# Performance work log

Hardware: AMD Instinct MI355X
Metric: run time of the kernel (lower is better)

Reference implementation:

```python
import jax, jax.numpy as jnp
import numpy as np

K = 20
NEG = 0.2      # leaky relu slope
EPS = 1e-5     # layernorm eps


def knn(x, k=K):
    # x: [B, C, N] -> neighbor indices [B, N, k] by largest negative sq-distance
    xt = jnp.swapaxes(x, 1, 2)                      # [B, N, C]
    inner = -2.0 * jnp.einsum('bnc,bcm->bnm', xt, x)
    xx = jnp.sum(x * x, axis=1)                     # [B, N]
    pd = -xx[:, :, None] - inner - xx[:, None, :]   # [B, N, N]
    _, idx = jax.lax.top_k(pd, k)
    return idx


def graph_feature(x, k=K):
    # x: [B, C, N] -> edge features [B, 2C, N, k] = cat(neighbor - center, center)
    xt = jnp.swapaxes(x, 1, 2)                      # [B, N, C]
    idx = knn(x, k)                                 # [B, N, k]
    nbr = jax.vmap(lambda f, i: f[i])(xt, idx)      # [B, N, k, C]
    ctr = jnp.broadcast_to(xt[:, :, None, :], nbr.shape)
    feat = jnp.concatenate([nbr - ctr, ctr], axis=-1)
    return jnp.transpose(feat, (0, 3, 1, 2))


def lrelu(x):
    return jnp.where(x >= 0, x, NEG * x)


def conv1x1(x, w):
    # x: [B, C, N, k], w: [O, C]  (BatchNorm2d in eval with default stats == identity)
    return jnp.einsum('oc,bcnk->bonk', w, x)


def layernorm(x, g, b):
    m = jnp.mean(x, axis=-1, keepdims=True)
    v = jnp.var(x, axis=-1, keepdims=True)
    return (x - m) * jax.lax.rsqrt(v + EPS) * g + b


def l2n(x):
    return x / jnp.linalg.norm(x, axis=1, keepdims=True)


def fc_layer(x, w, bias, g, beta):
    # l2-normalize -> Linear -> LayerNorm -> LeakyReLU (fc_layer with norm=True, bn=True)
    x = l2n(x)
    x = x @ w.T
    if bias is not None:
        x = x + bias
    return lrelu(layernorm(x, g, beta))


def transform_net(f0, tw1, tw2, tw3, tfc1_w, tfc1_g, tfc1_b, tfc2_w, tfc2_bias, tfc2_g, tfc2_b, tfc3_w, tfc3_b):
    # f0: [B, 6, N, k]
    h = lrelu(conv1x1(f0, tw1))                     # [B, 64, N, k]
    h = lrelu(conv1x1(h, tw2))                      # [B, 128, N, k]
    h = jnp.max(h, axis=-1, keepdims=True)          # [B, 128, N, 1]
    h = lrelu(conv1x1(h, tw3))                      # [B, 1024, N, 1]
    h = jnp.max(h, axis=2)[:, :, 0]                 # [B, 1024]
    h = fc_layer(h, tfc1_w, None, tfc1_g, tfc1_b)   # dgcnn: fc1 bias=False
    h = fc_layer(h, tfc2_w, tfc2_bias, tfc2_g, tfc2_b)
    h = h @ tfc3_w.T + tfc3_b                       # [B, 9]
    h = h + jnp.eye(3, dtype=h.dtype).reshape(9)
    return h.reshape(-1, 3, 3)


def setup_inputs() -> dict:
    key = jax.random.key(0)
    ks = jax.random.split(key, 16)

    def w(k, o, i):
        return jax.random.normal(k, (o, i), dtype=jnp.float32) / np.sqrt(i)

    inp = {
        'x': jax.random.normal(ks[0], (16, 3, 1024), dtype=jnp.float32),
        # transform_net params
        'tw1': w(ks[1], 64, 6),
        'tw2': w(ks[2], 128, 64),
        'tw3': w(ks[3], 1024, 128),
        'tfc1_w': w(ks[4], 512, 1024),
        'tfc1_g': jnp.ones((512,), jnp.float32),
        'tfc1_b': jnp.zeros((512,), jnp.float32),
        'tfc2_w': w(ks[5], 256, 512),
        'tfc2_bias': jnp.zeros((256,), jnp.float32),
        'tfc2_g': jnp.ones((256,), jnp.float32),
        'tfc2_b': jnp.zeros((256,), jnp.float32),
        'tfc3_w': w(ks[6], 9, 256) * 0.01,
        'tfc3_b': jnp.zeros((9,), jnp.float32),
        # EdgeConv params (1x1 convs, bias=False for dgcnn)
        'w1': w(ks[7], 64, 6),
        'w2': w(ks[8], 64, 128),
        'w3': w(ks[9], 128, 128),
        'w4': w(ks[10], 256, 256),
        'w5': w(ks[11], 1024, 512),
    }
    return inp


def reference(x, tw1, tw2, tw3, tfc1_w, tfc1_g, tfc1_b, tfc2_w, tfc2_bias, tfc2_g, tfc2_b,
              tfc3_w, tfc3_b, w1, w2, w3, w4, w5):
    # spatial transform from first graph feature
    f0 = graph_feature(x)                           # [B, 6, N, k]
    t = transform_net(f0, tw1, tw2, tw3, tfc1_w, tfc1_g, tfc1_b,
                      tfc2_w, tfc2_bias, tfc2_g, tfc2_b, tfc3_w, tfc3_b)
    x = jnp.einsum('bij,bjn->bin', t, x)            # [B, 3, N]

    # 4 EdgeConv blocks: graph_feature -> 1x1 conv (+BN identity) -> lrelu -> max over k
    x1 = jnp.max(lrelu(conv1x1(graph_feature(x), w1)), axis=-1)    # [B, 64, N]
    x2 = jnp.max(lrelu(conv1x1(graph_feature(x1), w2)), axis=-1)   # [B, 64, N]
    x3 = jnp.max(lrelu(conv1x1(graph_feature(x2), w3)), axis=-1)   # [B, 128, N]
    x4 = jnp.max(lrelu(conv1x1(graph_feature(x3), w4)), axis=-1)   # [B, 256, N]

    xc = jnp.concatenate([x1, x2, x3, x4], axis=1)  # [B, 512, N]
    x5 = lrelu(jnp.einsum('oc,bcn->bon', w5, xc))   # [B, 1024, N]
    return jnp.max(x5, axis=-1)                     # [B, 1024] global feature
```

## Files before the change

### kernel.cpp

```cpp
#include <hip/hip_runtime.h>
#include <math.h>

#define BATCH 16
#define NPTS 1024
#define KNN 20

__device__ __forceinline__ float lrelu(float v) { return v >= 0.f ? v : 0.2f * v; }

typedef __attribute__((ext_vector_type(8))) short bf16x8;
typedef __attribute__((ext_vector_type(4))) float f32x4;
typedef unsigned long long ull;

__device__ __forceinline__ ushort f2bf(float f) {
  union { float f; unsigned u; } v; v.f = f;
  unsigned r = (v.u + 0x7FFFu + ((v.u >> 16) & 1u)) >> 16;
  return (ushort)r;
}

__device__ __forceinline__ unsigned wave_min_u32(unsigned v) {
  unsigned t;
  t = (unsigned)__builtin_amdgcn_update_dpp((int)v, (int)v, 0x111, 0xf, 0xf, false);
  v = t < v ? t : v;
  t = (unsigned)__builtin_amdgcn_update_dpp((int)v, (int)v, 0x112, 0xf, 0xf, false);
  v = t < v ? t : v;
  t = (unsigned)__builtin_amdgcn_update_dpp((int)v, (int)v, 0x114, 0xf, 0xf, false);
  v = t < v ? t : v;
  t = (unsigned)__builtin_amdgcn_update_dpp((int)v, (int)v, 0x118, 0xf, 0xf, false);
  v = t < v ? t : v;
  t = (unsigned)__builtin_amdgcn_update_dpp((int)v, (int)v, 0x142, 0xf, 0xf, false);
  v = t < v ? t : v;
  t = (unsigned)__builtin_amdgcn_update_dpp((int)v, (int)v, 0x143, 0xf, 0xf, false);
  v = t < v ? t : v;
  return (unsigned)__builtin_amdgcn_readlane((int)v, 63);
}

__global__ __launch_bounds__(256)
void wsplit_t_kernel(const float* __restrict__ W, float* __restrict__ waT,
                     float* __restrict__ wdT, int O, int Cc) {
  int e = blockIdx.x * 256 + threadIdx.x;
  if (e < O * Cc) {
    int c = e / O, o = e - c * O;
    float a = W[o * 2 * Cc + c], bb = W[o * 2 * Cc + Cc + c];
    waT[e] = a; wdT[e] = bb - a;
  }
}

__global__ __launch_bounds__(256)
void wsplit_bf_kernel(const float* __restrict__ W, ushort* __restrict__ wa_bf,
                      ushort* __restrict__ wd_bf, int O, int Cc) {
  int e = blockIdx.x * 256 + threadIdx.x;
  if (e < O * Cc) {
    int o = e / Cc, c = e - o * Cc;
    float a = W[o * 2 * Cc + c], bb = W[o * 2 * Cc + Cc + c];
    wa_bf[e] = f2bf(a); wd_bf[e] = f2bf(bb - a);
  }
}

__global__ __launch_bounds__(256)
void cvt_bf16_kernel(const float* __restrict__ in, ushort* __restrict__ outp, int n) {
  int e = blockIdx.x * 256 + threadIdx.x;
  if (e < n) outp[e] = f2bf(in[e]);
}

__global__ __launch_bounds__(256)
void wtrans_kernel(const float* __restrict__ W, float* __restrict__ wT, int O, int Cc) {
  int e = blockIdx.x * 256 + threadIdx.x;
  if (e < O * Cc) {
    int c = e / O, o = e - c * O;
    wT[e] = W[(size_t)o * Cc + c];
  }
}

__global__ __launch_bounds__(256)
void xx3_kernel(const float* __restrict__ x, float* __restrict__ xx) {
  const int b = blockIdx.y;
  const int n = blockIdx.x * 256 + threadIdx.x;
  const float* xb = x + (size_t)b * 3 * NPTS;
  float a = xb[n], bb = xb[NPTS + n], c = xb[2 * NPTS + n];
  xx[b * NPTS + n] = a * a + bb * bb + c * c;
}

template<int C>
__global__ __launch_bounds__(256)
void knn_cn_kernel(const float* __restrict__ Xt, long sb,
                   const float* __restrict__ xx, int* __restrict__ idxout) {
  __shared__ float sc4[4][NPTS];
  const int b = blockIdx.y, i0 = blockIdx.x * 8;
  const int tid = threadIdx.x;
  const float* Xb = Xt + (size_t)b * sb;
  const int j0 = tid * 4;
  float acc[8][4];
  #pragma unroll
  for (int q = 0; q < 8; ++q)
    #pragma unroll
    for (int u = 0; u < 4; ++u) acc[q][u] = 0.f;
  for (int c = 0; c < C; ++c) {
    const float4 xv = *reinterpret_cast<const float4*>(Xb + (size_t)c * NPTS + j0);
    const float* xr = Xb + (size_t)c * NPTS + i0;
    #pragma unroll
    for (int q = 0; q < 8; ++q) {
      const float xiq = xr[q];
      acc[q][0] = fmaf(xiq, xv.x, acc[q][0]);
      acc[q][1] = fmaf(xiq, xv.y, acc[q][1]);
      acc[q][2] = fmaf(xiq, xv.z, acc[q][2]);
      acc[q][3] = fmaf(xiq, xv.w, acc[q][3]);
    }
  }
  const float4 xxj = *reinterpret_cast<const float4*>(xx + b * NPTS + j0);
  const int wv = tid >> 6, lane = tid & 63;
  unsigned ku0[16], ku1[16];

  #pragma unroll
  for (int q = 0; q < 4; ++q) {
    float4 st;
    st.x = fmaf(-2.f, acc[q][0], xxj.x);
    st.y = fmaf(-2.f, acc[q][1], xxj.y);
    st.z = fmaf(-2.f, acc[q][2], xxj.z);
    st.w = fmaf(-2.f, acc[q][3], xxj.w);
    *reinterpret_cast<float4*>(&sc4[q][j0]) = st;
  }
  __syncthreads();
  #pragma unroll
  for (int s = 0; s < 16; ++s) {
    const unsigned u = __float_as_uint(sc4[wv][lane + 64 * s]);
    ku0[s] = u ^ ((unsigned)((int)u >> 31) | 0x80000000u);
  }
  __syncthreads();
  #pragma unroll
  for (int q = 4; q < 8; ++q) {
    float4 st;
    st.x = fmaf(-2.f, acc[q][0], xxj.x);
    st.y = fmaf(-2.f, acc[q][1], xxj.y);
    st.z = fmaf(-2.f, acc[q][2], xxj.z);
    st.w = fmaf(-2.f, acc[q][3], xxj.w);
    *reinterpret_cast<float4*>(&sc4[q - 4][j0]) = st;
  }
  __syncthreads();
  #pragma unroll
  for (int s = 0; s < 16; ++s) {
    const unsigned u = __float_as_uint(sc4[wv][lane + 64 * s]);
    ku1[s] = u ^ ((unsigned)((int)u >> 31) | 0x80000000u);
  }

  unsigned b1v0 = 0xFFFFFFFFu, b2v0 = 0xFFFFFFFFu; int b1s0 = 0, b2s0 = 0;
  unsigned b1v1 = 0xFFFFFFFFu, b2v1 = 0xFFFFFFFFu; int b1s1 = 0, b2s1 = 0;
  #pragma unroll
  for (int s = 0; s < 16; ++s) {
    const unsigned s0 = ku0[s], s1 = ku1[s];
    const bool a1 = s0 < b1v0, a2 = s0 < b2v0;
    const unsigned na1 = a1 ? s0 : b1v0;  const int nas1 = a1 ? s : b1s0;
    const unsigned na2 = a1 ? b1v0 : (a2 ? s0 : b2v0);
    const int nas2 = a1 ? b1s0 : (a2 ? s : b2s0);
    b1v0 = na1; b1s0 = nas1; b2v0 = na2; b2s0 = nas2;
    const bool c1c = s1 < b1v1, c2c = s1 < b2v1;
    const unsigned nc1 = c1c ? s1 : b1v1;  const int ncs1 = c1c ? s : b1s1;
    const unsigned nc2 = c1c ? b1v1 : (c2c ? s1 : b2v1);
    const int ncs2 = c1c ? b1s1 : (c2c ? s : b2s1);
    b1v1 = nc1; b1s1 = ncs1; b2v1 = nc2; b2s1 = ncs2;
  }
  const unsigned INVS = 0xFFFFFFFFu;
  unsigned c1s0 = b1v0, c2s0 = b2v0;  int c1j0 = lane + (b1s0 << 6), c2j0 = lane + (b2s0 << 6);
  unsigned c1s1 = b1v1, c2s1 = b2v1;  int c1j1 = lane + (b1s1 << 6), c2j1 = lane + (b2s1 << 6);

  int my0 = 0, my1 = 0;
  for (int t = 0; t < KNN; ++t) {
    const unsigned ws0 = wave_min_u32(c1s0);
    const unsigned ws1 = wave_min_u32(c1s1);
    const int wl0 = __ffsll((long long)__ballot(c1s0 == ws0)) - 1;
    const int wl1 = __ffsll((long long)__ballot(c1s1 == ws1)) - 1;
    const int jw0 = __builtin_amdgcn_readlane(c1j0, wl0);
    const int jw1 = __builtin_amdgcn_readlane(c1j1, wl1);
    if (lane == t) { my0 = jw0; my1 = jw1; }
    const bool win0 = (lane == wl0), win1 = (lane == wl1);
    c1s0 = win0 ? c2s0 : c1s0;  c1j0 = win0 ? c2j0 : c1j0;  c2s0 = win0 ? INVS : c2s0;
    c1s1 = win1 ? c2s1 : c1s1;  c1j1 = win1 ? c2j1 : c1j1;  c2s1 = win1 ? INVS : c2s1;
    if (__any((c1s0 == INVS) || (c1s1 == INVS))) {
      if (c1s0 == INVS) {
        unsigned m1 = INVS, m2 = INVS; int r1 = 0, r2 = 0;
        #pragma unroll
        for (int s = 0; s < 16; ++s) {
          const unsigned k = ku0[s];
          const bool ok = k > ws0;
          const bool a1 = ok && (k < m1), a2 = ok && (k < m2);
          const unsigned nm1 = a1 ? k : m1;  const int nr1 = a1 ? s : r1;
          const unsigned nm2 = a1 ? m1 : (a2 ? k : m2);
          const int nr2 = a1 ? r1 : (a2 ? s : r2);
          m1 = nm1; r1 = nr1; m2 = nm2; r2 = nr2;
        }
        c1s0 = (m1 == INVS) ? 0xFFFFFFFEu : m1;  c1j0 = lane + (r1 << 6);
        c2s0 = (m2 == INVS) ? 0xFFFFFFFEu : m2;  c2j0 = lane + (r2 << 6);
      }
      if (c1s1 == INVS) {
        unsigned m1 = INVS, m2 = INVS; int r1 = 0, r2 = 0;
        #pragma unroll
        for (int s = 0; s < 16; ++s) {
          const unsigned k = ku1[s];
          const bool ok = k > ws1;
          const bool a1 = ok && (k < m1), a2 = ok && (k < m2);
          const unsigned nm1 = a1 ? k : m1;  const int nr1 = a1 ? s : r1;
          const unsigned nm2 = a1 ? m1 : (a2 ? k : m2);
          const int nr2 = a1 ? r1 : (a2 ? s : r2);
          m1 = nm1; r1 = nr1; m2 = nm2; r2 = nr2;
        }
        c1s1 = (m1 == INVS) ? 0xFFFFFFFEu : m1;  c1j1 = lane + (r1 << 6);
        c2s1 = (m2 == INVS) ? 0xFFFFFFFEu : m2;  c2j1 = lane + (r2 << 6);
      }
    }
  }
  if (lane < KNN) {
    idxout[(size_t)(b * NPTS + i0 + wv) * KNN + lane] = my0;
    idxout[(size_t)(b * NPTS + i0 + wv + 4) * KNN + lane] = my1;
  }
}

__global__ __launch_bounds__(256)
void gemm_kernel(const float* __restrict__ X, long sxb, int sxn, int sxc,
                 const float* __restrict__ WT, int ldW, int C,
                 float* __restrict__ out, int sob, int son) {
  __shared__ __align__(16) float Xs[16][64];
  __shared__ __align__(16) float Ws[16][64];
  const int b = blockIdx.z;
  const int n0 = blockIdx.x * 64, o0 = blockIdx.y * 64;
  const int tid = threadIdx.x;
  const int lr = tid & 63;
  const int c4 = (tid >> 6) * 4;
  const int tn = tid & 15, to = tid >> 4;
  float acc[4][4];
  #pragma unroll
  for (int i = 0; i < 4; ++i)
    #pragma unroll
    for (int j = 0; j < 4; ++j) acc[i][j] = 0.f;

  const size_t xbase = (size_t)b * sxb;
  for (int k0 = 0; k0 < C; k0 += 16) {
    #pragma unroll
    for (int u = 0; u < 4; ++u) {
      int c = k0 + c4 + u;
      float xv = 0.f, wv = 0.f;
      if (c < C) {
        xv = X[xbase + (size_t)(n0 + lr) * sxn + (size_t)c * sxc];
        wv = WT[(size_t)c * ldW + o0 + lr];
      }
      Xs[c4 + u][lr] = xv;
      Ws[c4 + u][lr] = wv;
    }
    __syncthreads();
    #pragma unroll
    for (int kk = 0; kk < 16; ++kk) {
      const float4 xa = *reinterpret_cast<const float4*>(&Xs[kk][tn * 4]);
      const float4 wb = *reinterpret_cast<const float4*>(&Ws[kk][to * 4]);
      const float xr[4] = {xa.x, xa.y, xa.z, xa.w};
      const float wr[4] = {wb.x, wb.y, wb.z, wb.w};
      #pragma unroll
      for (int i = 0; i < 4; ++i)
        #pragma unroll
        for (int j = 0; j < 4; ++j) acc[i][j] = fmaf(xr[i], wr[j], acc[i][j]);
    }
    __syncthreads();
  }
  #pragma unroll
  for (int i = 0; i < 4; ++i) {
    float4 st = make_float4(acc[i][0], acc[i][1], acc[i][2], acc[i][3]);
    *reinterpret_cast<float4*>(&out[(size_t)b * sob + (size_t)(n0 + tn * 4 + i) * son + o0 + to * 4]) = st;
  }
}

template<int EPI>
__global__ __launch_bounds__(256)
void gemm128_kernel(const float* __restrict__ X, long sxb, int scN,
                    const float* __restrict__ WT, int ldW, int C,
                    float* __restrict__ out, int sob, int son, int snb) {
  __shared__ __align__(16) float Xs[16][128];
  __shared__ __align__(16) float Ws[16][128];
  __shared__ __align__(16) float red[16][132];
  const int b = blockIdx.z;
  const int n0 = blockIdx.x * 128, o0 = blockIdx.y * 128;
  const int tid = threadIdx.x;
  const int tn = tid & 15, to = tid >> 4;
  float acc[8][8];
  #pragma unroll
  for (int i = 0; i < 8; ++i)
    #pragma unroll
    for (int j = 0; j < 8; ++j) acc[i][j] = 0.f;

  const size_t xbase = (size_t)b * sxb;
  for (int c0 = 0; c0 < C; c0 += 16) {
    #pragma unroll
    for (int it = 0; it < 2; ++it) {
      const int task = tid + it * 256;
      const int kk = task >> 5, n4 = (task & 31) * 4;
      *reinterpret_cast<float4*>(&Xs[kk][n4]) =
        *reinterpret_cast<const float4*>(&X[xbase + (size_t)(c0 + kk) * scN + n0 + n4]);
      *reinterpret_cast<float4*>(&Ws[kk][n4]) =
        *reinterpret_cast<const float4*>(&WT[(size_t)(c0 + kk) * ldW + o0 + n4]);
    }
    __syncthreads();
    #pragma unroll
    for (int kk = 0; kk < 16; ++kk) {
      const float4 xa0 = *reinterpret_cast<const float4*>(&Xs[kk][tn * 4]);
      const float4 xa1 = *reinterpret_cast<const float4*>(&Xs[kk][64 + tn * 4]);
      const float4 wb0 = *reinterpret_cast<const float4*>(&Ws[kk][to * 4]);
      const float4 wb1 = *reinterpret_cast<const float4*>(&Ws[kk][64 + to * 4]);
      const float xr[8] = {xa0.x, xa0.y, xa0.z, xa0.w, xa1.x, xa1.y, xa1.z, xa1.w};
      const float wr[8] = {wb0.x, wb0.y, wb0.z, wb0.w, wb1.x, wb1.y, wb1.z, wb1.w};
      #pragma unroll
      for (int i = 0; i < 8; ++i)
        #pragma unroll
        for (int j = 0; j < 8; ++j) acc[i][j] = fmaf(xr[i], wr[j], acc[i][j]);
    }
    __syncthreads();
  }

  if (EPI == 0) {
    #pragma unroll
    for (int i = 0; i < 8; ++i) {
      const int n = n0 + (i >> 2) * 64 + tn * 4 + (i & 3);
      float4 s0 = make_float4(acc[i][0], acc[i][1], acc[i][2], acc[i][3]);
      float4 s1 = make_float4(acc[i][4], acc[i][5], acc[i][6], acc[i][7]);
      *reinterpret_cast<float4*>(&out[(size_t)b * sob + (size_t)n * son + o0 + to * 4]) = s0;
      *reinterpret_cast<float4*>(&out[(size_t)b * sob + (size_t)n * son + o0 + 64 + to * 4]) = s1;
    }
  } else {
    #pragma unroll
    for (int j = 0; j < 8; ++j) {
      float m = lrelu(acc[0][j]);
      #pragma unroll
      for (int i = 1; i < 8; ++i) m = fmaxf(m, lrelu(acc[i][j]));
      red[tn][(j >> 2) * 64 + to * 4 + (j & 3)] = m;
    }
    __syncthreads();
    if (tid < 128) {
      float m = red[0][tid];
      #pragma unroll
      for (int t = 1; t < 16; ++t) m = fmaxf(m, red[t][tid]);
      out[(size_t)b * sob + (size_t)blockIdx.x * snb + o0 + tid] = m;
    }
  }
}

template<int EPI>
__global__ __launch_bounds__(256)
void gemm_mfma_kernel(const ushort* __restrict__ Xg, long sxb, int ldX,
                      const ushort* __restrict__ Wg, int ldW, int K,
                      float* __restrict__ out, long sob, int son, int snb) {
  __shared__ __align__(16) ushort As[128 * 64];
  __shared__ __align__(16) ushort Bs[128 * 64];
// ... 150 lines not shown
  #pragma unroll
  for (int it = 0; it < 5; ++it) {
    const int task = tid + it * 256;
    const int e = task >> 4, cq = (task & 15) * 4;
    const int p = e / KNN, t = e - p * KNN;
    const int j = idxs[p][t];
    const float4 yv = *reinterpret_cast<const float4*>(&ya[(size_t)(b * NPTS + j) * 64 + cq]);
    const float4 zv = *reinterpret_cast<const float4*>(&zbs[p][cq]);
    float4 hv;
    hv.x = lrelu(yv.x + zv.x); hv.y = lrelu(yv.y + zv.y);
    hv.z = lrelu(yv.z + zv.z); hv.w = lrelu(yv.w + zv.w);
    *reinterpret_cast<float4*>(&h1s[e][cq]) = hv;
  }
  __syncthreads();

  const int eg = tid >> 4, og = tid & 15;
  float acc[5][8];
  #pragma unroll
  for (int u = 0; u < 5; ++u)
    #pragma unroll
    for (int v = 0; v < 8; ++v) acc[u][v] = 0.f;
  #pragma unroll 4
  for (int kk = 0; kk < 64; ++kk) {
    float hv[5];
    #pragma unroll
    for (int u = 0; u < 5; ++u) hv[u] = h1s[eg * 5 + u][kk];
    const float4 w0 = *reinterpret_cast<const float4*>(&ws[kk][og * 4]);
    const float4 w1 = *reinterpret_cast<const float4*>(&ws[kk][64 + og * 4]);
    const float wr[8] = {w0.x, w0.y, w0.z, w0.w, w1.x, w1.y, w1.z, w1.w};
    #pragma unroll
    for (int u = 0; u < 5; ++u)
      #pragma unroll
      for (int v = 0; v < 8; ++v) acc[u][v] = fmaf(hv[u], wr[v], acc[u][v]);
  }

  const int p = eg >> 2, d = eg & 3;
  float m[8];
  #pragma unroll
  for (int v = 0; v < 8; ++v) {
    float mm = lrelu(acc[0][v]);
    #pragma unroll
    for (int u = 1; u < 5; ++u) mm = fmaxf(mm, lrelu(acc[u][v]));
    mm = fmaxf(mm, __shfl_xor(mm, 16));
    mm = fmaxf(mm, __shfl_xor(mm, 32));
    m[v] = mm;
  }
  if (d == 0) {
    #pragma unroll
    for (int v = 0; v < 8; ++v) {
      const int o = og * 4 + (v & 3) + (v >> 2) * 64;
      ot[o][p] = m[v];
    }
  }
  __syncthreads();
  if (tid < 128) {
    float4 st = make_float4(ot[tid][0], ot[tid][1], ot[tid][2], ot[tid][3]);
    *reinterpret_cast<float4*>(&h2m[(size_t)(b * 128 + tid) * NPTS + i0]) = st;
  }
}

__global__ __launch_bounds__(256)
void reduce_max_kernel(const float* __restrict__ part, float* __restrict__ outp, int nt) {
  const int b = blockIdx.y;
  const int o = blockIdx.x * 256 + threadIdx.x;
  float m = part[(size_t)(b * nt) * 1024 + o];
  for (int t = 1; t < nt; ++t) m = fmaxf(m, part[(size_t)(b * nt + t) * 1024 + o]);
  outp[b * 1024 + o] = m;
}

__device__ __forceinline__ float block_reduce_sum(float v, float* rbuf) {
  #pragma unroll
  for (int off = 32; off > 0; off >>= 1) v += __shfl_xor(v, off);
  const int w = threadIdx.x >> 6, lane = threadIdx.x & 63;
  const int nw = blockDim.x >> 6;
  if (lane == 0) rbuf[w] = v;
  __syncthreads();
  float tot = 0.f;
  for (int i = 0; i < nw; ++i) tot += rbuf[i];
  __syncthreads();
  return tot;
}

__global__ __launch_bounds__(256)
void fc1_kernel(const float* __restrict__ gin_g, const float* __restrict__ Wt,
                const float* __restrict__ gam, const float* __restrict__ bet,
                float* __restrict__ outp) {
  __shared__ __align__(16) float gin[1024];
  __shared__ float hbuf[512];
  __shared__ float rbuf[8];
  const int b = blockIdx.x, tid = threadIdx.x;
  for (int e = tid; e < 1024; e += 256) gin[e] = gin_g[b * 1024 + e];
  __syncthreads();
  float ps = 0.f;
  for (int e = tid; e < 1024; e += 256) ps = fmaf(gin[e], gin[e], ps);
  float ss = block_reduce_sum(ps, rbuf);
  float rinv = 1.0f / sqrtf(ss);
  #pragma unroll
  for (int r = 0; r < 2; ++r) {
    int o = tid + r * 256;
    const float* wrow = Wt + (size_t)o * 1024;
    float a = 0.f;
    for (int c4 = 0; c4 < 256; ++c4) {
      float4 wv = *reinterpret_cast<const float4*>(wrow + c4 * 4);
      float4 gv = *reinterpret_cast<const float4*>(&gin[c4 * 4]);
      a = fmaf(wv.x, gv.x, a); a = fmaf(wv.y, gv.y, a);
      a = fmaf(wv.z, gv.z, a); a = fmaf(wv.w, gv.w, a);
    }
    hbuf[o] = a * rinv;
  }
  __syncthreads();
  float pm = hbuf[tid] + hbuf[tid + 256];
  float mean = block_reduce_sum(pm, rbuf) * (1.f / 512.f);
  float d0 = hbuf[tid] - mean, d1 = hbuf[tid + 256] - mean;
  float var = block_reduce_sum(d0 * d0 + d1 * d1, rbuf) * (1.f / 512.f);
  float rs = 1.0f / sqrtf(var + 1e-5f);
  #pragma unroll
  for (int r = 0; r < 2; ++r) {
    int o = tid + r * 256;
    float yv = (hbuf[o] - mean) * rs * gam[o] + bet[o];
    outp[b * 512 + o] = lrelu(yv);
  }
}

__global__ __launch_bounds__(256)
void fc2_kernel(const float* __restrict__ inp, const float* __restrict__ Wt,
                const float* __restrict__ bias, const float* __restrict__ gam,
                const float* __restrict__ bet, float* __restrict__ outp) {
  __shared__ __align__(16) float gin[512];
  __shared__ float rbuf[8];
  const int b = blockIdx.x, tid = threadIdx.x;
  for (int e = tid; e < 512; e += 256) gin[e] = inp[b * 512 + e];
  __syncthreads();
  float ps = 0.f;
  for (int e = tid; e < 512; e += 256) ps = fmaf(gin[e], gin[e], ps);
  float ss = block_reduce_sum(ps, rbuf);
  float rinv = 1.0f / sqrtf(ss);
  const float* wrow = Wt + (size_t)tid * 512;
  float a = 0.f;
  for (int c4 = 0; c4 < 128; ++c4) {
    float4 wv = *reinterpret_cast<const float4*>(wrow + c4 * 4);
    float4 gv = *reinterpret_cast<const float4*>(&gin[c4 * 4]);
    a = fmaf(wv.x, gv.x, a); a = fmaf(wv.y, gv.y, a);
    a = fmaf(wv.z, gv.z, a); a = fmaf(wv.w, gv.w, a);
  }
  a = a * rinv + bias[tid];
  float mean = block_reduce_sum(a, rbuf) * (1.f / 256.f);
  float d = a - mean;
  float var = block_reduce_sum(d * d, rbuf) * (1.f / 256.f);
  float rs = 1.0f / sqrtf(var + 1e-5f);
  float yv = (a - mean) * rs * gam[tid] + bet[tid];
  outp[b * 256 + tid] = lrelu(yv);
}

__global__ __launch_bounds__(64)
void fc3_kernel(const float* __restrict__ inp, const float* __restrict__ Wt,
                const float* __restrict__ bias, float* __restrict__ tmat) {
  __shared__ float gin[256];
  const int b = blockIdx.x, tid = threadIdx.x;
  for (int e = tid; e < 256; e += 64) gin[e] = inp[b * 256 + e];
  __syncthreads();
  if (tid < 9) {
    const float* wrow = Wt + tid * 256;
    float a = 0.f;
    for (int c = 0; c < 256; ++c) a = fmaf(wrow[c], gin[c], a);
    a += bias[tid];
    if (tid == 0 || tid == 4 || tid == 8) a += 1.f;
    tmat[b * 9 + tid] = a;
  }
}

__global__ __launch_bounds__(256)
void xform_kernel(const float* __restrict__ x, const float* __restrict__ tmat,
                  float* __restrict__ xt) {
  const int b = blockIdx.y;
  const int n = blockIdx.x * 256 + threadIdx.x;
  const float* xb = x + (size_t)b * 3 * NPTS;
  const float x0 = xb[n], x1 = xb[NPTS + n], x2 = xb[2 * NPTS + n];
  const float* t = tmat + b * 9;
  float* ob = xt + (size_t)b * 3 * NPTS;
  #pragma unroll
  for (int i = 0; i < 3; ++i)
    ob[i * NPTS + n] = fmaf(t[3 * i], x0, fmaf(t[3 * i + 1], x1, t[3 * i + 2] * x2));
}

extern "C" void kernel_launch(void* const* d_in, const int* in_sizes, int n_in,
                              void* d_out, int out_size, void* d_ws, size_t ws_size,
                              hipStream_t stream) {
  (void)in_sizes; (void)n_in; (void)out_size; (void)ws_size;
  const float* x       = (const float*)d_in[0];
  const float* tw1     = (const float*)d_in[1];
  const float* tw2     = (const float*)d_in[2];
  const float* tw3     = (const float*)d_in[3];
  const float* tfc1_w  = (const float*)d_in[4];
  const float* tfc1_g  = (const float*)d_in[5];
  const float* tfc1_b  = (const float*)d_in[6];
  const float* tfc2_w  = (const float*)d_in[7];
  const float* tfc2_bias = (const float*)d_in[8];
  const float* tfc2_g  = (const float*)d_in[9];
  const float* tfc2_b  = (const float*)d_in[10];
  const float* tfc3_w  = (const float*)d_in[11];
  const float* tfc3_b  = (const float*)d_in[12];
  const float* w1      = (const float*)d_in[13];
  const float* w2      = (const float*)d_in[14];
  const float* w3      = (const float*)d_in[15];
  const float* w4      = (const float*)d_in[16];
  const float* w5      = (const float*)d_in[17];
  float* out = (float*)d_out;

  char* wsb = (char*)d_ws;
  size_t off = 0;
  auto alloc = [&](size_t bytes) -> void* {
    void* p = wsb + off;
    off += (bytes + 255) & ~(size_t)255;
    return p;
  };
  float* ybuf = (float*)alloc((size_t)BATCH * NPTS * 256 * 4);
  float* zbuf = (float*)alloc((size_t)BATCH * NPTS * 256 * 4);
  float* xcT  = (float*)alloc((size_t)BATCH * 512 * NPTS * 4);
  ushort* xc_bf = (ushort*)alloc((size_t)BATCH * NPTS * 512 * 2);
  float* h2m  = (float*)alloc((size_t)BATCH * 128 * NPTS * 4);
  float* part = (float*)alloc((size_t)BATCH * 16 * 1024 * 4);
  int*   idxb = (int*)alloc((size_t)BATCH * NPTS * KNN * 4);
  float* xxb  = (float*)alloc((size_t)BATCH * NPTS * 4);
  float* xt   = (float*)alloc((size_t)BATCH * 3 * NPTS * 4);
  float* gbuf = (float*)alloc((size_t)BATCH * 1024 * 4);
  float* f1o  = (float*)alloc((size_t)BATCH * 512 * 4);
  float* f2o  = (float*)alloc((size_t)BATCH * 256 * 4);
  float* tmat = (float*)alloc((size_t)BATCH * 9 * 4);
  float* tw1aT = (float*)alloc(3 * 64 * 4);
  float* tw1dT = (float*)alloc(3 * 64 * 4);
  float* w1aT  = (float*)alloc(3 * 64 * 4);
  float* w1dT  = (float*)alloc(3 * 64 * 4);
  float* w2aT  = (float*)alloc(64 * 64 * 4);
  float* w2dT  = (float*)alloc(64 * 64 * 4);
  float* w3aT  = (float*)alloc(64 * 128 * 4);
  float* w3dT  = (float*)alloc(64 * 128 * 4);
  ushort* w4a_bf = (ushort*)alloc(256 * 128 * 2);
  ushort* w4d_bf = (ushort*)alloc(256 * 128 * 2);
  ushort* w5_bf  = (ushort*)alloc(1024 * 512 * 2);
  float* tw2T  = (float*)alloc(64 * 128 * 4);
  float* tw3T  = (float*)alloc(128 * 1024 * 4);

  wsplit_t_kernel<<<1, 256, 0, stream>>>(tw1, tw1aT, tw1dT, 64, 3);
  wsplit_t_kernel<<<1, 256, 0, stream>>>(w1, w1aT, w1dT, 64, 3);
  wsplit_t_kernel<<<16, 256, 0, stream>>>(w2, w2aT, w2dT, 64, 64);
  wsplit_t_kernel<<<32, 256, 0, stream>>>(w3, w3aT, w3dT, 128, 64);
  wsplit_bf_kernel<<<128, 256, 0, stream>>>(w4, w4a_bf, w4d_bf, 256, 128);
  cvt_bf16_kernel<<<2048, 256, 0, stream>>>(w5, w5_bf, 1024 * 512);
  wtrans_kernel<<<32, 256, 0, stream>>>(tw2, tw2T, 128, 64);
  wtrans_kernel<<<512, 256, 0, stream>>>(tw3, tw3T, 1024, 128);

  xx3_kernel<<<dim3(4, 16), 256, 0, stream>>>(x, xxb);
  knn_cn_kernel<3><<<dim3(128, 16), 256, 0, stream>>>(x, 3 * NPTS, xxb, idxb);
  gemm_kernel<<<dim3(16, 1, 16), 256, 0, stream>>>(x, 3 * NPTS, 1, NPTS, tw1aT, 64, 3,
                                                   ybuf, NPTS * 64, 64);
  gemm_kernel<<<dim3(16, 1, 16), 256, 0, stream>>>(x, 3 * NPTS, 1, NPTS, tw1dT, 64, 3,
                                                   zbuf, NPTS * 64, 64);
  h12_gemm_kernel<<<dim3(256, 16), 256, 0, stream>>>(ybuf, zbuf, idxb, tw2T, h2m);
  gemm128_kernel<1><<<dim3(8, 8, 16), 256, 0, stream>>>(h2m, 128 * NPTS, NPTS, tw3T, 1024, 128,
                                                        part, 8 * 1024, 0, 1024);
  reduce_max_kernel<<<dim3(4, 16), 256, 0, stream>>>(part, gbuf, 8);
  fc1_kernel<<<16, 256, 0, stream>>>(gbuf, tfc1_w, tfc1_g, tfc1_b, f1o);
  fc2_kernel<<<16, 256, 0, stream>>>(f1o, tfc2_w, tfc2_bias, tfc2_g, tfc2_b, f2o);
  fc3_kernel<<<16, 64, 0, stream>>>(f2o, tfc3_w, tfc3_b, tmat);
  xform_kernel<<<dim3(4, 16), 256, 0, stream>>>(x, tmat, xt);

  xx3_kernel<<<dim3(4, 16), 256, 0, stream>>>(xt, xxb);
  knn_cn_kernel<3><<<dim3(128, 16), 256, 0, stream>>>(xt, 3 * NPTS, xxb, idxb);
  gemm_kernel<<<dim3(16, 1, 16), 256, 0, stream>>>(xt, 3 * NPTS, 1, NPTS, w1aT, 64, 3,
                                                   ybuf, NPTS * 64, 64);
  gemm_kernel<<<dim3(16, 1, 16), 256, 0, stream>>>(xt, 3 * NPTS, 1, NPTS, w1dT, 64, 3,
                                                   zbuf, NPTS * 64, 64);
  edge_max_cn_kernel<64, 64><<<dim3(16, 16), 256, 0, stream>>>(ybuf, zbuf, idxb, xcT, xxb,
                                                               xc_bf, 0);

  knn_cn_kernel<64><<<dim3(128, 16), 256, 0, stream>>>(xcT, 512 * NPTS, xxb, idxb);
  gemm_kernel<<<dim3(16, 1, 16), 256, 0, stream>>>(xcT, 512 * NPTS, 1, NPTS, w2aT, 64, 64,
                                                   ybuf, NPTS * 64, 64);
  gemm_kernel<<<dim3(16, 1, 16), 256, 0, stream>>>(xcT, 512 * NPTS, 1, NPTS, w2dT, 64, 64,
                                                   zbuf, NPTS * 64, 64);
  edge_max_cn_kernel<64, 64><<<dim3(16, 16), 256, 0, stream>>>(ybuf, zbuf, idxb,
                                                               xcT + 64 * NPTS, xxb, xc_bf, 64);

  knn_cn_kernel<64><<<dim3(128, 16), 256, 0, stream>>>(xcT + 64 * NPTS, 512 * NPTS, xxb, idxb);
  gemm_kernel<<<dim3(16, 2, 16), 256, 0, stream>>>(xcT + 64 * NPTS, 512 * NPTS, 1, NPTS,
                                                   w3aT, 128, 64, ybuf, NPTS * 128, 128);
  gemm_kernel<<<dim3(16, 2, 16), 256, 0, stream>>>(xcT + 64 * NPTS, 512 * NPTS, 1, NPTS,
                                                   w3dT, 128, 64, zbuf, NPTS * 128, 128);
  edge_max_cn_kernel<128, 64><<<dim3(16, 16), 256, 0, stream>>>(ybuf, zbuf, idxb,
                                                                xcT + 128 * NPTS, xxb, xc_bf, 128);

  knn_cn_kernel<128><<<dim3(128, 16), 256, 0, stream>>>(xcT + 128 * NPTS, 512 * NPTS, xxb, idxb);
  gemm_mfma_kernel<0><<<dim3(8, 2, 16), 256, 0, stream>>>(xc_bf + 128, (long)NPTS * 512, 512,
                                                          w4a_bf, 128, 128,
                                                          ybuf, (long)NPTS * 256, 256, 0);
  gemm_mfma_kernel<0><<<dim3(8, 2, 16), 256, 0, stream>>>(xc_bf + 128, (long)NPTS * 512, 512,
                                                          w4d_bf, 128, 128,
                                                          zbuf, (long)NPTS * 256, 256, 0);
  edge_max_cn_kernel<256, 32><<<dim3(32, 16), 256, 0, stream>>>(ybuf, zbuf, idxb,
                                                                xcT + 256 * NPTS, nullptr,
                                                                xc_bf, 256);

  gemm_mfma_kernel<1><<<dim3(8, 8, 16), 256, 0, stream>>>(xc_bf, (long)NPTS * 512, 512,
                                                          w5_bf, 512, 512,
                                                          part, 8 * 1024, 0, 1024);
  reduce_max_kernel<<<dim3(4, 16), 256, 0, stream>>>(part, out, 8);
}
```

Before: 755.4 us.

## Widen kNN tile to 16 rows, fuse dual 1x1 GEMMs and FC chain

```diff
diff --git a/kernel.cpp b/kernel.cpp
--- a/kernel.cpp
+++ b/kernel.cpp
@@ -85,20 +85,20 @@
 void knn_cn_kernel(const float* __restrict__ Xt, long sb,
                    const float* __restrict__ xx, int* __restrict__ idxout) {
   __shared__ float sc4[4][NPTS];
-  const int b = blockIdx.y, i0 = blockIdx.x * 8;
+  const int b = blockIdx.y, i0 = blockIdx.x * 16;
   const int tid = threadIdx.x;
   const float* Xb = Xt + (size_t)b * sb;
   const int j0 = tid * 4;
-  float acc[8][4];
-  #pragma unroll
-  for (int q = 0; q < 8; ++q)
+  float acc[16][4];
+  #pragma unroll
+  for (int q = 0; q < 16; ++q)
     #pragma unroll
     for (int u = 0; u < 4; ++u) acc[q][u] = 0.f;
   for (int c = 0; c < C; ++c) {
     const float4 xv = *reinterpret_cast<const float4*>(Xb + (size_t)c * NPTS + j0);
     const float* xr = Xb + (size_t)c * NPTS + i0;
     #pragma unroll
-    for (int q = 0; q < 8; ++q) {
+    for (int q = 0; q < 16; ++q) {
       const float xiq = xr[q];
       acc[q][0] = fmaf(xiq, xv.x, acc[q][0]);
       acc[q][1] = fmaf(xiq, xv.y, acc[q][1]);
@@ -108,160 +108,158 @@
   }
   const float4 xxj = *reinterpret_cast<const float4*>(xx + b * NPTS + j0);
   const int wv = tid >> 6, lane = tid & 63;
-  unsigned ku0[16], ku1[16];
-
-  #pragma unroll
-  for (int q = 0; q < 4; ++q) {
-    float4 st;
-    st.x = fmaf(-2.f, acc[q][0], xxj.x);
-    st.y = fmaf(-2.f, acc[q][1], xxj.y);
-    st.z = fmaf(-2.f, acc[q][2], xxj.z);
-    st.w = fmaf(-2.f, acc[q][3], xxj.w);
-    *reinterpret_cast<float4*>(&sc4[q][j0]) = st;
-  }
-  __syncthreads();
-  #pragma unroll
-  for (int s = 0; s < 16; ++s) {
-    const unsigned u = __float_as_uint(sc4[wv][lane + 64 * s]);
-    ku0[s] = u ^ ((unsigned)((int)u >> 31) | 0x80000000u);
-  }
-  __syncthreads();
-  #pragma unroll
-  for (int q = 4; q < 8; ++q) {
-    float4 st;
-    st.x = fmaf(-2.f, acc[q][0], xxj.x);
-    st.y = fmaf(-2.f, acc[q][1], xxj.y);
-    st.z = fmaf(-2.f, acc[q][2], xxj.z);
-    st.w = fmaf(-2.f, acc[q][3], xxj.w);
-    *reinterpret_cast<float4*>(&sc4[q - 4][j0]) = st;
-  }
-  __syncthreads();
-  #pragma unroll
-  for (int s = 0; s < 16; ++s) {
-    const unsigned u = __float_as_uint(sc4[wv][lane + 64 * s]);
-    ku1[s] = u ^ ((unsigned)((int)u >> 31) | 0x80000000u);
-  }
-
-  unsigned b1v0 = 0xFFFFFFFFu, b2v0 = 0xFFFFFFFFu; int b1s0 = 0, b2s0 = 0;
-  unsigned b1v1 = 0xFFFFFFFFu, b2v1 = 0xFFFFFFFFu; int b1s1 = 0, b2s1 = 0;
-  #pragma unroll
-  for (int s = 0; s < 16; ++s) {
-    const unsigned s0 = ku0[s], s1 = ku1[s];
-    const bool a1 = s0 < b1v0, a2 = s0 < b2v0;
-    const unsigned na1 = a1 ? s0 : b1v0;  const int nas1 = a1 ? s : b1s0;
-    const unsigned na2 = a1 ? b1v0 : (a2 ? s0 : b2v0);
-    const int nas2 = a1 ? b1s0 : (a2 ? s : b2s0);
-    b1v0 = na1; b1s0 = nas1; b2v0 = na2; b2s0 = nas2;
-    const bool c1c = s1 < b1v1, c2c = s1 < b2v1;
-    const unsigned nc1 = c1c ? s1 : b1v1;  const int ncs1 = c1c ? s : b1s1;
-    const unsigned nc2 = c1c ? b1v1 : (c2c ? s1 : b2v1);
-    const int ncs2 = c1c ? b1s1 : (c2c ? s : b2s1);
-    b1v1 = nc1; b1s1 = ncs1; b2v1 = nc2; b2s1 = ncs2;
+  unsigned ku[4][16];
+
+  #pragma unroll
+  for (int r = 0; r < 4; ++r) {
+    if (r > 0) __syncthreads();
+    #pragma unroll
+    for (int q = 0; q < 4; ++q) {
+      const int qq = r * 4 + q;
+      float4 st;
+      st.x = fmaf(-2.f, acc[qq][0], xxj.x);
+      st.y = fmaf(-2.f, acc[qq][1], xxj.y);
+      st.z = fmaf(-2.f, acc[qq][2], xxj.z);
+      st.w = fmaf(-2.f, acc[qq][3], xxj.w);
+      *reinterpret_cast<float4*>(&sc4[q][j0]) = st;
+    }
+    __syncthreads();
+    #pragma unroll
+    for (int s = 0; s < 16; ++s) {
+      const unsigned u = __float_as_uint(sc4[wv][lane + 64 * s]);
+      ku[r][s] = u ^ ((unsigned)((int)u >> 31) | 0x80000000u);
+    }
+  }
+
+  unsigned c1s[4], c2s[4]; int c1j[4], c2j[4];
+  #pragma unroll
+  for (int r = 0; r < 4; ++r) {
+    unsigned b1 = 0xFFFFFFFFu, b2 = 0xFFFFFFFFu; int s1 = 0, s2 = 0;
+    #pragma unroll
+    for (int s = 0; s < 16; ++s) {
+      const unsigned k = ku[r][s];
+      const bool a1 = k < b1, a2 = k < b2;
+      const unsigned n1 = a1 ? k : b1;  const int ns1 = a1 ? s : s1;
+      const unsigned n2 = a1 ? b1 : (a2 ? k : b2);
+      const int ns2 = a1 ? s1 : (a2 ? s : s2);
+      b1 = n1; s1 = ns1; b2 = n2; s2 = ns2;
+    }
+    c1s[r] = b1; c1j[r] = lane + (s1 << 6);
+    c2s[r] = b2; c2j[r] = lane + (s2 << 6);
   }
   const unsigned INVS = 0xFFFFFFFFu;
-  unsigned c1s0 = b1v0, c2s0 = b2v0;  int c1j0 = lane + (b1s0 << 6), c2j0 = lane + (b2s0 << 6);
-  unsigned c1s1 = b1v1, c2s1 = b2v1;  int c1j1 = lane + (b1s1 << 6), c2j1 = lane + (b2s1 << 6);
-
-  int my0 = 0, my1 = 0;
+  int my[4] = {0, 0, 0, 0};
   for (int t = 0; t < KNN; ++t) {
-    const unsigned ws0 = wave_min_u32(c1s0);
-    const unsigned ws1 = wave_min_u32(c1s1);
-    const int wl0 = __ffsll((long long)__ballot(c1s0 == ws0)) - 1;
-    const int wl1 = __ffsll((long long)__ballot(c1s1 == ws1)) - 1;
-    const int jw0 = __builtin_amdgcn_readlane(c1j0, wl0);
-    const int jw1 = __builtin_amdgcn_readlane(c1j1, wl1);
-    if (lane == t) { my0 = jw0; my1 = jw1; }
-    const bool win0 = (lane == wl0), win1 = (lane == wl1);
-    c1s0 = win0 ? c2s0 : c1s0;  c1j0 = win0 ? c2j0 : c1j0;  c2s0 = win0 ? INVS : c2s0;
-    c1s1 = win1 ? c2s1 : c1s1;  c1j1 = win1 ? c2j1 : c1j1;  c2s1 = win1 ? INVS : c2s1;
-    if (__any((c1s0 == INVS) || (c1s1 == INVS))) {
-      if (c1s0 == INVS) {
-        unsigned m1 = INVS, m2 = INVS; int r1 = 0, r2 = 0;
-        #pragma unroll
-        for (int s = 0; s < 16; ++s) {
-          const unsigned k = ku0[s];
-          const bool ok = k > ws0;
-          const bool a1 = ok && (k < m1), a2 = ok && (k < m2);
-          const unsigned nm1 = a1 ? k : m1;  const int nr1 = a1 ? s : r1;
-          const unsigned nm2 = a1 ? m1 : (a2 ? k : m2);
-          const int nr2 = a1 ? r1 : (a2 ? s : r2);
-          m1 = nm1; r1 = nr1; m2 = nm2; r2 = nr2;
+    unsigned ws[4]; int wl[4], jw[4];
+    #pragma unroll
+    for (int r = 0; r < 4; ++r) ws[r] = wave_min_u32(c1s[r]);
+    #pragma unroll
+    for (int r = 0; r < 4; ++r) wl[r] = __ffsll((long long)__ballot(c1s[r] == ws[r])) - 1;
+    #pragma unroll
+    for (int r = 0; r < 4; ++r) jw[r] = __builtin_amdgcn_readlane(c1j[r], wl[r]);
+    if (lane == t) {
+      #pragma unroll
+      for (int r = 0; r < 4; ++r) my[r] = jw[r];
+    }
+    bool cons = false;
+    #pragma unroll
+    for (int r = 0; r < 4; ++r) {
+      const bool win = (lane == wl[r]);
+      c1s[r] = win ? c2s[r] : c1s[r];
+      c1j[r] = win ? c2j[r] : c1j[r];
+      c2s[r] = win ? INVS : c2s[r];
+      cons = cons || (c1s[r] == INVS);
+    }
+    if (__any(cons)) {
+      #pragma unroll
+      for (int r = 0; r < 4; ++r) {
+        if (c1s[r] == INVS) {
+          unsigned m1 = INVS, m2 = INVS; int r1 = 0, r2 = 0;
+          #pragma unroll
+          for (int s = 0; s < 16; ++s) {
+            const unsigned k = ku[r][s];
+            const bool ok = k > ws[r];
+            const bool a1 = ok && (k < m1), a2 = ok && (k < m2);
+            const unsigned nm1 = a1 ? k : m1;  const int nr1 = a1 ? s : r1;
+            const unsigned nm2 = a1 ? m1 : (a2 ? k : m2);
+            const int nr2 = a1 ? r1 : (a2 ? s : r2);
+            m1 = nm1; r1 = nr1; m2 = nm2; r2 = nr2;
+          }
+          c1s[r] = (m1 == INVS) ? 0xFFFFFFFEu : m1;  c1j[r] = lane + (r1 << 6);
+          c2s[r] = (m2 == INVS) ? 0xFFFFFFFEu : m2;  c2j[r] = lane + (r2 << 6);
         }
-        c1s0 = (m1 == INVS) ? 0xFFFFFFFEu : m1;  c1j0 = lane + (r1 << 6);
-        c2s0 = (m2 == INVS) ? 0xFFFFFFFEu : m2;  c2j0 = lane + (r2 << 6);
       }
-      if (c1s1 == INVS) {
-        unsigned m1 = INVS, m2 = INVS; int r1 = 0, r2 = 0;
-        #pragma unroll
-        for (int s = 0; s < 16; ++s) {
-          const unsigned k = ku1[s];
-          const bool ok = k > ws1;
-          const bool a1 = ok && (k < m1), a2 = ok && (k < m2);
-          const unsigned nm1 = a1 ? k : m1;  const int nr1 = a1 ? s : r1;
-          const unsigned nm2 = a1 ? m1 : (a2 ? k : m2);
-          const int nr2 = a1 ? r1 : (a2 ? s : r2);
-          m1 = nm1; r1 = nr1; m2 = nm2; r2 = nr2;
-        }
-        c1s1 = (m1 == INVS) ? 0xFFFFFFFEu : m1;  c1j1 = lane + (r1 << 6);
-        c2s1 = (m2 == INVS) ? 0xFFFFFFFEu : m2;  c2j1 = lane + (r2 << 6);
-      }
     }
   }
   if (lane < KNN) {
-    idxout[(size_t)(b * NPTS + i0 + wv) * KNN + lane] = my0;
-    idxout[(size_t)(b * NPTS + i0 + wv + 4) * KNN + lane] = my1;
-  }
-}
-
-__global__ __launch_bounds__(256)
-void gemm_kernel(const float* __restrict__ X, long sxb, int sxn, int sxc,
-                 const float* __restrict__ WT, int ldW, int C,
-                 float* __restrict__ out, int sob, int son) {
+    #pragma unroll
+    for (int r = 0; r < 4; ++r)
+      idxout[(size_t)(b * NPTS + i0 + r * 4 + wv) * KNN + lane] = my[r];
+  }
+}
+
+__global__ __launch_bounds__(256)
+void gemm_dual_kernel(const float* __restrict__ X, long sxb, int sxn, int sxc,
+                      const float* __restrict__ WaT, const float* __restrict__ WdT,
+                      int ldW, int C,
+                      float* __restrict__ outY, float* __restrict__ outZ,
+                      int sob, int son) {
   __shared__ __align__(16) float Xs[16][64];
-  __shared__ __align__(16) float Ws[16][64];
+  __shared__ __align__(16) float Was[16][64];
+  __shared__ __align__(16) float Wds[16][64];
   const int b = blockIdx.z;
   const int n0 = blockIdx.x * 64, o0 = blockIdx.y * 64;
   const int tid = threadIdx.x;
   const int lr = tid & 63;
   const int c4 = (tid >> 6) * 4;
   const int tn = tid & 15, to = tid >> 4;
-  float acc[4][4];
+  float accY[4][4], accZ[4][4];
   #pragma unroll
   for (int i = 0; i < 4; ++i)
     #pragma unroll
-    for (int j = 0; j < 4; ++j) acc[i][j] = 0.f;
+    for (int j = 0; j < 4; ++j) { accY[i][j] = 0.f; accZ[i][j] = 0.f; }
 
   const size_t xbase = (size_t)b * sxb;
   for (int k0 = 0; k0 < C; k0 += 16) {
     #pragma unroll
     for (int u = 0; u < 4; ++u) {
       int c = k0 + c4 + u;
-      float xv = 0.f, wv = 0.f;
+      float xv = 0.f, wa = 0.f, wd = 0.f;
       if (c < C) {
         xv = X[xbase + (size_t)(n0 + lr) * sxn + (size_t)c * sxc];
-        wv = WT[(size_t)c * ldW + o0 + lr];
+        wa = WaT[(size_t)c * ldW + o0 + lr];
+        wd = WdT[(size_t)c * ldW + o0 + lr];
       }
       Xs[c4 + u][lr] = xv;
-      Ws[c4 + u][lr] = wv;
+      Was[c4 + u][lr] = wa;
+      Wds[c4 + u][lr] = wd;
     }
     __syncthreads();
     #pragma unroll
     for (int kk = 0; kk < 16; ++kk) {
       const float4 xa = *reinterpret_cast<const float4*>(&Xs[kk][tn * 4]);
-      const float4 wb = *reinterpret_cast<const float4*>(&Ws[kk][to * 4]);
+      const float4 wav = *reinterpret_cast<const float4*>(&Was[kk][to * 4]);
+      const float4 wdv = *reinterpret_cast<const float4*>(&Wds[kk][to * 4]);
       const float xr[4] = {xa.x, xa.y, xa.z, xa.w};
-      const float wr[4] = {wb.x, wb.y, wb.z, wb.w};
+      const float war[4] = {wav.x, wav.y, wav.z, wav.w};
+      const float wdr[4] = {wdv.x, wdv.y, wdv.z, wdv.w};
       #pragma unroll
       for (int i = 0; i < 4; ++i)
         #pragma unroll
-        for (int j = 0; j < 4; ++j) acc[i][j] = fmaf(xr[i], wr[j], acc[i][j]);
+        for (int j = 0; j < 4; ++j) {
+          accY[i][j] = fmaf(xr[i], war[j], accY[i][j]);
+          accZ[i][j] = fmaf(xr[i], wdr[j], accZ[i][j]);
+        }
     }
     __syncthreads();
   }
   #pragma unroll
   for (int i = 0; i < 4; ++i) {
-    float4 st = make_float4(acc[i][0], acc[i][1], acc[i][2], acc[i][3]);
-    *reinterpret_cast<float4*>(&out[(size_t)b * sob + (size_t)(n0 + tn * 4 + i) * son + o0 + to * 4]) = st;
+    const size_t base = (size_t)b * sob + (size_t)(n0 + tn * 4 + i) * son + o0 + to * 4;
+    *reinterpret_cast<float4*>(&outY[base]) =
+      make_float4(accY[i][0], accY[i][1], accY[i][2], accY[i][3]);
+    *reinterpret_cast<float4*>(&outZ[base]) =
+      make_float4(accZ[i][0], accZ[i][1], accZ[i][2], accZ[i][3]);
   }
 }
 
@@ -578,14 +576,27 @@
 }
 
 __global__ __launch_bounds__(256)
-void fc1_kernel(const float* __restrict__ gin_g, const float* __restrict__ Wt,
-                const float* __restrict__ gam, const float* __restrict__ bet,
-                float* __restrict__ outp) {
+void fcall_kernel(const float* __restrict__ part,
+                  const float* __restrict__ Wt1, const float* __restrict__ g1,
+                  const float* __restrict__ bb1,
+                  const float* __restrict__ Wt2, const float* __restrict__ bias2,
+                  const float* __restrict__ g2, const float* __restrict__ bb2,
+                  const float* __restrict__ Wt3, const float* __restrict__ bb3,
+                  const float* __restrict__ x, float* __restrict__ xt) {
   __shared__ __align__(16) float gin[1024];
+  __shared__ __align__(16) float f1s[512];
+  __shared__ float f2s[256];
   __shared__ float hbuf[512];
   __shared__ float rbuf[8];
+  __shared__ float tm[9];
   const int b = blockIdx.x, tid = threadIdx.x;
-  for (int e = tid; e < 1024; e += 256) gin[e] = gin_g[b * 1024 + e];
+  for (int e = tid; e < 1024; e += 256) {
+    const float* pp = part + (size_t)b * 8192 + e;
+    float m = pp[0];
+    #pragma unroll
+    for (int t = 1; t < 8; ++t) m = fmaxf(m, pp[t * 1024]);
+    gin[e] = m;
+  }
   __syncthreads();
   float ps = 0.f;
   for (int e = tid; e < 1024; e += 256) ps = fmaf(gin[e], gin[e], ps);
@@ -594,7 +605,7 @@
   #pragma unroll
   for (int r = 0; r < 2; ++r) {
     int o = tid + r * 256;
-    const float* wrow = Wt + (size_t)o * 1024;
+    const float* wrow = Wt1 + (size_t)o * 1024;
     float a = 0.f;
     for (int c4 = 0; c4 < 256; ++c4) {
       float4 wv = *reinterpret_cast<const float4*>(wrow + c4 * 4);
@@ -613,70 +624,47 @@
   #pragma unroll
   for (int r = 0; r < 2; ++r) {
     int o = tid + r * 256;
-    float yv = (hbuf[o] - mean) * rs * gam[o] + bet[o];
-    outp[b * 512 + o] = lrelu(yv);
-  }
-}
-
-__global__ __launch_bounds__(256)
-void fc2_kernel(const float* __restrict__ inp, const float* __restrict__ Wt,
-                const float* __restrict__ bias, const float* __restrict__ gam,
-                const float* __restrict__ bet, float* __restrict__ outp) {
-  __shared__ __align__(16) float gin[512];
-  __shared__ float rbuf[8];
-  const int b = blockIdx.x, tid = threadIdx.x;
-  for (int e = tid; e < 512; e += 256) gin[e] = inp[b * 512 + e];
-  __syncthreads();
-  float ps = 0.f;
-  for (int e = tid; e < 512; e += 256) ps = fmaf(gin[e], gin[e], ps);
-  float ss = block_reduce_sum(ps, rbuf);
-  float rinv = 1.0f / sqrtf(ss);
-  const float* wrow = Wt + (size_t)tid * 512;
-  float a = 0.f;
+    f1s[o] = lrelu((hbuf[o] - mean) * rs * g1[o] + bb1[o]);
+  }
+  __syncthreads();
+  float ps2 = 0.f;
+  for (int e = tid; e < 512; e += 256) ps2 = fmaf(f1s[e], f1s[e], ps2);
+  float ss2 = block_reduce_sum(ps2, rbuf);
+  float rinv2 = 1.0f / sqrtf(ss2);
+  const float* wrow2 = Wt2 + (size_t)tid * 512;
+  float a2 = 0.f;
   for (int c4 = 0; c4 < 128; ++c4) {
-    float4 wv = *reinterpret_cast<const float4*>(wrow + c4 * 4);
-    float4 gv = *reinterpret_cast<const float4*>(&gin[c4 * 4]);
-    a = fmaf(wv.x, gv.x, a); a = fmaf(wv.y, gv.y, a);
-    a = fmaf(wv.z, gv.z, a); a = fmaf(wv.w, gv.w, a);
-  }
-  a = a * rinv + bias[tid];
-  float mean = block_reduce_sum(a, rbuf) * (1.f / 256.f);
-  float d = a - mean;
-  float var = block_reduce_sum(d * d, rbuf) * (1.f / 256.f);
-  float rs = 1.0f / sqrtf(var + 1e-5f);
-  float yv = (a - mean) * rs * gam[tid] + bet[tid];
-  outp[b * 256 + tid] = lrelu(yv);
-}
-
-__global__ __launch_bounds__(64)
-void fc3_kernel(const float* __restrict__ inp, const float* __restrict__ Wt,
-                const float* __restrict__ bias, float* __restrict__ tmat) {
-  __shared__ float gin[256];
-  const int b = blockIdx.x, tid = threadIdx.x;
-  for (int e = tid; e < 256; e += 64) gin[e] = inp[b * 256 + e];
+    float4 wv = *reinterpret_cast<const float4*>(wrow2 + c4 * 4);
+    float4 gv = *reinterpret_cast<const float4*>(&f1s[c4 * 4]);
+    a2 = fmaf(wv.x, gv.x, a2); a2 = fmaf(wv.y, gv.y, a2);
+    a2 = fmaf(wv.z, gv.z, a2); a2 = fmaf(wv.w, gv.w, a2);
+  }
+  a2 = a2 * rinv2 + bias2[tid];
+  float mean2 = block_reduce_sum(a2, rbuf) * (1.f / 256.f);
+  float dd = a2 - mean2;
+  float var2 = block_reduce_sum(dd * dd, rbuf) * (1.f / 256.f);
+  float rs2 = 1.0f / sqrtf(var2 + 1e-5f);
+  f2s[tid] = lrelu((a2 - mean2) * rs2 * g2[tid] + bb2[tid]);
   __syncthreads();
   if (tid < 9) {
-    const float* wrow = Wt + tid * 256;
-    float a = 0.f;
-    for (int c = 0; c < 256; ++c) a = fmaf(wrow[c], gin[c], a);
-    a += bias[tid];
-    if (tid == 0 || tid == 4 || tid == 8) a += 1.f;
-    tmat[b * 9 + tid] = a;
-  }
-}
-
-__global__ __launch_bounds__(256)
-void xform_kernel(const float* __restrict__ x, const float* __restrict__ tmat,
-                  float* __restrict__ xt) {
-  const int b = blockIdx.y;
-  const int n = blockIdx.x * 256 + threadIdx.x;
+    const float* wrow3 = Wt3 + tid * 256;
+    float a3 = 0.f;
+    for (int c = 0; c < 256; ++c) a3 = fmaf(wrow3[c], f2s[c], a3);
+    a3 += bb3[tid];
+    if (tid == 0 || tid == 4 || tid == 8) a3 += 1.f;
+    tm[tid] = a3;
+  }
+  __syncthreads();
   const float* xb = x + (size_t)b * 3 * NPTS;
-  const float x0 = xb[n], x1 = xb[NPTS + n], x2 = xb[2 * NPTS + n];
-  const float* t = tmat + b * 9;
   float* ob = xt + (size_t)b * 3 * NPTS;
   #pragma unroll
-  for (int i = 0; i < 3; ++i)
-    ob[i * NPTS + n] = fmaf(t[3 * i], x0, fmaf(t[3 * i + 1], x1, t[3 * i + 2] * x2));
+  for (int nt = 0; nt < 4; ++nt) {
+    const int n = nt * 256 + tid;
+    const float x0 = xb[n], x1 = xb[NPTS + n], x2 = xb[2 * NPTS + n];
+    #pragma unroll
+    for (int i = 0; i < 3; ++i)
+      ob[i * NPTS + n] = fmaf(tm[3 * i], x0, fmaf(tm[3 * i + 1], x1, tm[3 * i + 2] * x2));
+  }
 }
 
 extern "C" void kernel_launch(void* const* d_in, const int* in_sizes, int n_in,
@@ -719,10 +707,6 @@
   int*   idxb = (int*)alloc((size_t)BATCH * NPTS * KNN * 4);
   float* xxb  = (float*)alloc((size_t)BATCH * NPTS * 4);
   float* xt   = (float*)alloc((size_t)BATCH * 3 * NPTS * 4);
-  float* gbuf = (float*)alloc((size_t)BATCH * 1024 * 4);
-  float* f1o  = (float*)alloc((size_t)BATCH * 512 * 4);
-  float* f2o  = (float*)alloc((size_t)BATCH * 256 * 4);
-  float* tmat = (float*)alloc((size_t)BATCH * 9 * 4);
   float* tw1aT = (float*)alloc(3 * 64 * 4);
   float* tw1dT = (float*)alloc(3 * 64 * 4);
   float* w1aT  = (float*)alloc(3 * 64 * 4);
@@ -747,46 +731,37 @@
   wtrans_kernel<<<512, 256, 0, stream>>>(tw3, tw3T, 1024, 128);
 
   xx3_kernel<<<dim3(4, 16), 256, 0, stream>>>(x, xxb);
-  knn_cn_kernel<3><<<dim3(128, 16), 256, 0, stream>>>(x, 3 * NPTS, xxb, idxb);
-  gemm_kernel<<<dim3(16, 1, 16), 256, 0, stream>>>(x, 3 * NPTS, 1, NPTS, tw1aT, 64, 3,
-                                                   ybuf, NPTS * 64, 64);
-  gemm_kernel<<<dim3(16, 1, 16), 256, 0, stream>>>(x, 3 * NPTS, 1, NPTS, tw1dT, 64, 3,
-                                                   zbuf, NPTS * 64, 64);
+  knn_cn_kernel<3><<<dim3(64, 16), 256, 0, stream>>>(x, 3 * NPTS, xxb, idxb);
+  gemm_dual_kernel<<<dim3(16, 1, 16), 256, 0, stream>>>(x, 3 * NPTS, 1, NPTS, tw1aT, tw1dT,
+                                                        64, 3, ybuf, zbuf, NPTS * 64, 64);
   h12_gemm_kernel<<<dim3(256, 16), 256, 0, stream>>>(ybuf, zbuf, idxb, tw2T, h2m);
   gemm128_kernel<1><<<dim3(8, 8, 16), 256, 0, stream>>>(h2m, 128 * NPTS, NPTS, tw3T, 1024, 128,
                                                         part, 8 * 1024, 0, 1024);
-  reduce_max_kernel<<<dim3(4, 16), 256, 0, stream>>>(part, gbuf, 8);
-  fc1_kernel<<<16, 256, 0, stream>>>(gbuf, tfc1_w, tfc1_g, tfc1_b, f1o);
-  fc2_kernel<<<16, 256, 0, stream>>>(f1o, tfc2_w, tfc2_bias, tfc2_g, tfc2_b, f2o);
-  fc3_kernel<<<16, 64, 0, stream>>>(f2o, tfc3_w, tfc3_b, tmat);
-  xform_kernel<<<dim3(4, 16), 256, 0, stream>>>(x, tmat, xt);
+  fcall_kernel<<<16, 256, 0, stream>>>(part, tfc1_w, tfc1_g, tfc1_b,
+                                       tfc2_w, tfc2_bias, tfc2_g, tfc2_b,
+                                       tfc3_w, tfc3_b, x, xt);
 
   xx3_kernel<<<dim3(4, 16), 256, 0, stream>>>(xt, xxb);
-  knn_cn_kernel<3><<<dim3(128, 16), 256, 0, stream>>>(xt, 3 * NPTS, xxb, idxb);
-  gemm_kernel<<<dim3(16, 1, 16), 256, 0, stream>>>(xt, 3 * NPTS, 1, NPTS, w1aT, 64, 3,
-                                                   ybuf, NPTS * 64, 64);
-  gemm_kernel<<<dim3(16, 1, 16), 256, 0, stream>>>(xt, 3 * NPTS, 1, NPTS, w1dT, 64, 3,
-                                                   zbuf, NPTS * 64, 64);
+  knn_cn_kernel<3><<<dim3(64, 16), 256, 0, stream>>>(xt, 3 * NPTS, xxb, idxb);
+  gemm_dual_kernel<<<dim3(16, 1, 16), 256, 0, stream>>>(xt, 3 * NPTS, 1, NPTS, w1aT, w1dT,
+                                                        64, 3, ybuf, zbuf, NPTS * 64, 64);
   edge_max_cn_kernel<64, 64><<<dim3(16, 16), 256, 0, stream>>>(ybuf, zbuf, idxb, xcT, xxb,
                                                                xc_bf, 0);
 
-  knn_cn_kernel<64><<<dim3(128, 16), 256, 0, stream>>>(xcT, 512 * NPTS, xxb, idxb);
-  gemm_kernel<<<dim3(16, 1, 16), 256, 0, stream>>>(xcT, 512 * NPTS, 1, NPTS, w2aT, 64, 64,
-                                                   ybuf, NPTS * 64, 64);
-  gemm_kernel<<<dim3(16, 1, 16), 256, 0, stream>>>(xcT, 512 * NPTS, 1, NPTS, w2dT, 64, 64,
-                                                   zbuf, NPTS * 64, 64);
+  knn_cn_kernel<64><<<dim3(64, 16), 256, 0, stream>>>(xcT, 512 * NPTS, xxb, idxb);
+  gemm_dual_kernel<<<dim3(16, 1, 16), 256, 0, stream>>>(xcT, 512 * NPTS, 1, NPTS, w2aT, w2dT,
+                                                        64, 64, ybuf, zbuf, NPTS * 64, 64);
   edge_max_cn_kernel<64, 64><<<dim3(16, 16), 256, 0, stream>>>(ybuf, zbuf, idxb,
                                                                xcT + 64 * NPTS, xxb, xc_bf, 64);
 
-  knn_cn_kernel<64><<<dim3(128, 16), 256, 0, stream>>>(xcT + 64 * NPTS, 512 * NPTS, xxb, idxb);
-  gemm_kernel<<<dim3(16, 2, 16), 256, 0, stream>>>(xcT + 64 * NPTS, 512 * NPTS, 1, NPTS,
-                                                   w3aT, 128, 64, ybuf, NPTS * 128, 128);
-  gemm_kernel<<<dim3(16, 2, 16), 256, 0, stream>>>(xcT + 64 * NPTS, 512 * NPTS, 1, NPTS,
-                                                   w3dT, 128, 64, zbuf, NPTS * 128, 128);
+  knn_cn_kernel<64><<<dim3(64, 16), 256, 0, stream>>>(xcT + 64 * NPTS, 512 * NPTS, xxb, idxb);
+  gemm_dual_kernel<<<dim3(16, 2, 16), 256, 0, stream>>>(xcT + 64 * NPTS, 512 * NPTS, 1, NPTS,
+                                                        w3aT, w3dT, 128, 64,
+                                                        ybuf, zbuf, NPTS * 128, 128);
   edge_max_cn_kernel<128, 64><<<dim3(16, 16), 256, 0, stream>>>(ybuf, zbuf, idxb,
                                                                 xcT + 128 * NPTS, xxb, xc_bf, 128);
 
-  knn_cn_kernel<128><<<dim3(128, 16), 256, 0, stream>>>(xcT + 128 * NPTS, 512 * NPTS, xxb, idxb);
+  knn_cn_kernel<128><<<dim3(64, 16), 256, 0, stream>>>(xcT + 128 * NPTS, 512 * NPTS, xxb, idxb);
   gemm_mfma_kernel<0><<<dim3(8, 2, 16), 256, 0, stream>>>(xc_bf + 128, (long)NPTS * 512, 512,
                                                           w4a_bf, 128, 128,
                                                           ybuf, (long)NPTS * 256, 256, 0);
```

After: 734.9 us. 1.03x faster.
